# Kernel optimization log

Measured on AMD Instinct MI355X. Metric: run time of the kernel, lower is better.

The kernel has to match this reference:

```python
import jax, jax.numpy as jnp
import numpy as np

B, H, V, DEPTH = 64, 1024, 32000, 5


def setup_inputs() -> dict:
    key = jax.random.key(0)
    ks = jax.random.split(key, 9)
    s = 1.0 / np.sqrt(H)
    u = lambda k, shape: jax.random.uniform(k, shape, jnp.float32, -s, s)
    return {
        "encoding": jax.random.normal(ks[0], (B, H), jnp.float32),
        "Whh_l": u(ks[1], (3 * H, H)),
        "bih_l": u(ks[2], (3 * H,)),
        "bhh_l": u(ks[3], (3 * H,)),
        "Whh_r": u(ks[4], (3 * H, H)),
        "bih_r": u(ks[5], (3 * H,)),
        "bhh_r": u(ks[6], (3 * H,)),
        "W_out": u(ks[7], (V, H)),
        "b_out": u(ks[8], (V,)),
        "depth": DEPTH,
    }


def _gru_zero_input(h, Whh, bih, bhh):
    # PyTorch GRU cell with x == 0: W_ih @ x vanishes, only b_ih survives.
    d = h.shape[-1]
    gh = h @ Whh.T + bhh                                   # [N, 3H]
    r = jax.nn.sigmoid(bih[:d] + gh[..., :d])
    z = jax.nn.sigmoid(bih[d:2 * d] + gh[..., d:2 * d])
    n = jnp.tanh(bih[2 * d:] + r * gh[..., 2 * d:])
    return (1.0 - z) * n + z * h


def reference(encoding, Whh_l, bih_l, bhh_l, Whh_r, bih_r, bhh_r, W_out, b_out, depth):
    b, h = encoding.shape
    cur = encoding[:, None, :]                             # [B, 1, H] roots
    for _ in range(depth):                                 # expand perfect binary tree, level-batched
        n = cur.shape[1]
        flat = cur.reshape(b * n, h)
        left = _gru_zero_input(flat, Whh_l, bih_l, bhh_l).reshape(b, n, h)
        right = _gru_zero_input(flat, Whh_r, bih_r, bhh_r).reshape(b, n, h)
        cur = jnp.stack([left, right], axis=2).reshape(b, 2 * n, h)  # interleave children
    logits = jnp.einsum("blh,vh->blv", cur, W_out) + b_out  # [B, L, V]
    return jax.nn.log_softmax(logits, axis=-1)
```

## Files before the change

### kernel.cpp

```cpp
#include <hip/hip_runtime.h>
#include <hip/hip_bf16.h>
#include <cstdint>
#include <cstddef>

#define H_DIM   1024
#define B_DIM   64
#define V_DIM   32000
#define DEPTH_C 5

using bf16x8  = __attribute__((ext_vector_type(8))) __bf16;
using bf16x4  = __attribute__((ext_vector_type(4))) __bf16;
using floatx4 = __attribute__((ext_vector_type(4))) float;

__device__ __forceinline__ void gl_lds16(const __bf16* g, __bf16* l) {
  __builtin_amdgcn_global_load_lds(
      (const __attribute__((address_space(1))) unsigned int*)g,
      (__attribute__((address_space(3))) unsigned int*)l, 16, 0, 0);
}

__global__ __launch_bounds__(256) void f2b(const float* __restrict__ in,
                                           __bf16* __restrict__ out, int n) {
  for (int i = (blockIdx.x * 256 + threadIdx.x) * 4; i < n;
       i += gridDim.x * 1024) {
    float4 v = *(const float4*)(in + i);
    bf16x4 o;
    o[0] = (__bf16)v.x; o[1] = (__bf16)v.y; o[2] = (__bf16)v.z; o[3] = (__bf16)v.w;
    *(bf16x4*)(out + i) = o;
  }
}

__device__ __forceinline__ bf16x8 cvt8(float4 a, float4 b) {
  bf16x8 r;
  r[0] = (__bf16)a.x; r[1] = (__bf16)a.y; r[2] = (__bf16)a.z; r[3] = (__bf16)a.w;
  r[4] = (__bf16)b.x; r[5] = (__bf16)b.y; r[6] = (__bf16)b.z; r[7] = (__bf16)b.w;
  return r;
}

#define VMCNT(n) asm volatile("s_waitcnt vmcnt(" #n ")" ::: "memory")
#define LGK0()                                  \
  do {                                          \
    asm volatile("s_waitcnt lgkmcnt(0)" ::: "memory"); \
    __builtin_amdgcn_sched_barrier(0);          \
  } while (0)
#define SBAR()                                  \
  do {                                          \
    __builtin_amdgcn_sched_barrier(0);          \
    __builtin_amdgcn_s_barrier();               \
    __builtin_amdgcn_sched_barrier(0);          \
  } while (0)
#define LDA(MH, KS)                                                          \
  do {                                                                       \
    _Pragma("unroll") for (int mf = 0; mf < 4; ++mf)                         \
        aF[mf] = *(const bf16x8*)(cb + aRow + (MH)*8192 + mf * 2048 +        \
                                  ((KS) ? cksw1 : cksw0));                   \
  } while (0)
#define LDB(KS)                                                              \
  do {                                                                       \
    _Pragma("unroll") for (int nj = 0; nj < 4; ++nj)                         \
        bB[nj] = *(const bf16x8*)(cb + 32768 + bRow + nj * 2048 +            \
                                  ((KS) ? cksw1 : cksw0));                   \
  } while (0)
#define MM(MH)                                                               \
  do {                                                                       \
    __builtin_amdgcn_s_setprio(1);                                           \
    _Pragma("unroll") for (int mf = 0; mf < 4; ++mf)                         \
        _Pragma("unroll") for (int nj = 0; nj < 4; ++nj)                     \
            acc[(MH)*4 + mf][nj] = __builtin_amdgcn_mfma_f32_16x16x32_bf16(  \
                aF[mf], bB[nj], acc[(MH)*4 + mf][nj], 0, 0, 0);              \
    __builtin_amdgcn_s_setprio(0);                                           \
  } while (0)

__global__ __launch_bounds__(512, 2) void gemm_logits_8ph(
    const __bf16* __restrict__ A, const __bf16* __restrict__ Wb,
    float* __restrict__ Cf, const float* __restrict__ bias,
    float2* __restrict__ part) {
  __shared__ __align__(16) char smem[131072];

  const int tid = threadIdx.x;
  int h = blockIdx.y * 8 + blockIdx.x;
  h = (h & 7) * 125 + (h >> 3);
  const int bx = h & 7, by = h >> 3;
  const int m0 = bx * 256, n0 = by * 256;

  const int lane = tid & 63, wave = tid >> 6;
  const int wr = wave >> 2, wc = wave & 3;
  const int lrow = lane & 15, quad = lane >> 4;

  const int aRow  = (wr * 128 + lrow) * 128;
  const int bRow  = (wc * 64 + lrow) * 128;
  const int lsw   = (lrow & 7) << 4;
  const int cksw0 = (quad * 16) ^ lsw;
  const int cksw1 = (64 + quad * 16) ^ lsw;

  const int t8  = tid >> 3;
  const int cix = (tid & 7) ^ (t8 & 7);
  const __bf16* gA00 = A + (size_t)(m0 + t8) * 1024 + cix * 8;
  const __bf16* gA01 = A + (size_t)(m0 + 128 + t8) * 1024 + cix * 8;
  const __bf16* gA10 = gA00 + 64 * 1024;
  const __bf16* gA11 = gA01 + 64 * 1024;
  const __bf16* gB00 = Wb + (size_t)(n0 + t8) * 1024 + cix * 8;
  const __bf16* gB01 = Wb + (size_t)(n0 + 64 + t8) * 1024 + cix * 8;
  const __bf16* gB10 = gB00 + 128 * 1024;
  const __bf16* gB11 = gB01 + 128 * 1024;

  floatx4 acc[8][4] = {};
  bf16x8 aF[4], bB[4];

  gl_lds16(gA00, (__bf16*)(smem + tid * 16));
  gl_lds16(gA01, (__bf16*)(smem + 16384 + tid * 16));
  gl_lds16(gB00, (__bf16*)(smem + 32768 + tid * 16));
  gl_lds16(gB01, (__bf16*)(smem + 40960 + tid * 16));
  gl_lds16(gB10, (__bf16*)(smem + 49152 + tid * 16));
  gl_lds16(gB11, (__bf16*)(smem + 57344 + tid * 16));
  gl_lds16(gA10, (__bf16*)(smem + 8192 + tid * 16));
  gl_lds16(gA11, (__bf16*)(smem + 24576 + tid * 16));
  VMCNT(2);
  SBAR();

  for (int t = 0; t < 15; ++t) {
    char* cb = smem + (t & 1) * 65536;
    char* nb = smem + ((t & 1) ^ 1) * 65536;
    const int ke = (t + 1) * 64;
    LDB(0); LDA(0, 0);
    gl_lds16(gA00 + ke, (__bf16*)(nb + tid * 16));
    gl_lds16(gA01 + ke, (__bf16*)(nb + 16384 + tid * 16));
    SBAR(); LGK0();
    MM(0);
    VMCNT(2); SBAR();
    LDA(1, 0);
    gl_lds16(gB00 + ke, (__bf16*)(nb + 32768 + tid * 16));
    gl_lds16(gB01 + ke, (__bf16*)(nb + 40960 + tid * 16));
    SBAR(); LGK0();
    MM(1);
    SBAR();
    LDB(1); LDA(0, 1);
    gl_lds16(gB10 + ke, (__bf16*)(nb + 49152 + tid * 16));
    gl_lds16(gB11 + ke, (__bf16*)(nb + 57344 + tid * 16));
    SBAR(); LGK0();
    MM(0);
    SBAR();
    LDA(1, 1);
    gl_lds16(gA10 + ke, (__bf16*)(nb + 8192 + tid * 16));
    gl_lds16(gA11 + ke, (__bf16*)(nb + 24576 + tid * 16));
    SBAR(); LGK0();
    MM(1);
    VMCNT(2); SBAR();
  }
  {
    char* cb = smem + 65536;
    LDB(0); LDA(0, 0); MM(0);
    VMCNT(0); SBAR();
    LDA(1, 0); MM(1);
    LDB(1); LDA(0, 1); MM(0);
    LDA(1, 1); MM(1);
  }

  float bv[4];
#pragma unroll
  for (int nj = 0; nj < 4; ++nj) bv[nj] = bias[n0 + wc * 64 + nj * 16 + lrow];

  float* lf = (float*)smem;

  __syncthreads();
#pragma unroll
  for (int half = 0; half < 2; ++half) {
    if (half) __syncthreads();
    if (wr == half) {
#pragma unroll
      for (int mi = 0; mi < 8; ++mi) {
#pragma unroll
        for (int nj = 0; nj < 4; ++nj) {
          const int colg = wc * 16 + nj * 4 + (lrow >> 2);
          const int cole = lrow & 3;
#pragma unroll
          for (int r = 0; r < 4; ++r) {
            const int rowL = mi * 16 + quad * 4 + r;
            lf[rowL * 256 + ((colg ^ (rowL & 7)) << 2) + cole] =
                acc[mi][nj][r] + bv[nj];
          }
        }
      }
    }
    __syncthreads();
#pragma unroll
    for (int it = 0; it < 16; ++it) {
      const int rowL = it * 8 + wave;
      const int rsw  = rowL & 7;
      const float4 v =
          *(const float4*)&lf[rowL * 256 + ((lane ^ rsw) << 2)];
      const int grow = m0 + half * 128 + rowL;
      *(float4*)(Cf + (size_t)grow * V_DIM + n0 + lane * 4) = v;
      float mx = fmaxf(fmaxf(v.x, v.y), fmaxf(v.z, v.w));
#pragma unroll
      for (int off = 32; off; off >>= 1) mx = fmaxf(mx, __shfl_xor(mx, off, 64));
      float sm = __expf(v.x - mx) + __expf(v.y - mx) + __expf(v.z - mx) +
                 __expf(v.w - mx);
#pragma unroll
      for (int off = 32; off; off >>= 1) sm += __shfl_xor(sm, off, 64);
      if (lane == 0)
        part[(size_t)grow * gridDim.y + by] = make_float2(mx, sm);
    }
  }
}

__global__ __launch_bounds__(256) void gemm_tree(
    const __bf16* __restrict__ A, const __bf16* __restrict__ Wb0,
    const __bf16* __restrict__ Wb1, __bf16* __restrict__ Cb, int M) {
  constexpr int K = H_DIM;
  __shared__ __align__(16) __bf16 As[3][128 * 32];
  __shared__ __align__(16) __bf16 Bs[3][64 * 32];

  const int tid = threadIdx.x;
  const int nbx = gridDim.x;
  const int nwg = nbx * gridDim.y;
  int hflat = blockIdx.y * nbx + blockIdx.x;
  if ((nwg & 7) == 0) {
    const int cpx = nwg >> 3;
    hflat = (hflat & 7) * cpx + (hflat >> 3);
  }
  const int bx = hflat % nbx;
  const int by = hflat / nbx;
  const int m0 = bx * 128;
  const int n0 = by * 64;
  const int lane = tid & 63, wave = tid >> 6;
  const int lrow = lane & 15, quad = lane >> 4;
  const int wm = wave * 32;

  const __bf16* Wb = Wb0;
  int nw0 = n0;
  if (n0 >= 3072) { Wb = Wb1; nw0 = n0 - 3072; }

  const int sr = tid >> 2;
  const int sk = (tid & 3) * 8;
  int ra0 = m0 + sr;      if (ra0 >= M) ra0 = M - 1;
  int ra1 = m0 + sr + 64; if (ra1 >= M) ra1 = M - 1;
  const __bf16* ga0 = A + (size_t)ra0 * K + sk;
  const __bf16* ga1 = A + (size_t)ra1 * K + sk;
  const __bf16* gb0 = Wb + (size_t)(nw0 + sr) * K + sk;

  floatx4 acc[2][4] = {};

#define TSTAGE(T, BUF)                                     \
  do {                                                     \
    gl_lds16(ga0 + (T) * 32, As[BUF] + tid * 8);           \
    gl_lds16(ga1 + (T) * 32, As[BUF] + 2048 + tid * 8);    \
    gl_lds16(gb0 + (T) * 32, Bs[BUF] + tid * 8);           \
  } while (0)
#define TCOMP(CB)                                                            \
  do {                                                                       \
    bf16x8 af[2], bfr[4];                                                    \
    _Pragma("unroll") for (int i = 0; i < 2; i++)                            \
        af[i] = *(const bf16x8*)(&As[CB][(wm + i * 16 + lrow) * 32 +         \
                                         quad * 8]);                         \
    _Pragma("unroll") for (int j = 0; j < 4; j++)                            \
        bfr[j] = *(const bf16x8*)(&Bs[CB][(j * 16 + lrow) * 32 + quad * 8]); \
    _Pragma("unroll") for (int i = 0; i < 2; i++)                            \
        _Pragma("unroll") for (int j = 0; j < 4; j++)                        \
            acc[i][j] = __builtin_amdgcn_mfma_f32_16x16x32_bf16(             \
                af[i], bfr[j], acc[i][j], 0, 0, 0);                          \
  } while (0)

  TSTAGE(0, 0);
  TSTAGE(1, 1);
  for (int t = 0; t < 31; ++t) {
    VMCNT(3);
    SBAR();
    if (t + 2 < 32) TSTAGE(t + 2, (t + 2) % 3);
    TCOMP(t % 3);
  }
  VMCNT(0);
  SBAR();
  TCOMP(31 % 3);
#undef TSTAGE
#undef TCOMP

#pragma unroll
  for (int i = 0; i < 2; i++) {
#pragma unroll
    for (int j = 0; j < 4; j++) {
      const int col = n0 + j * 16 + lrow;
#pragma unroll
      for (int r = 0; r < 4; r++) {
        const int row = m0 + wm + i * 16 + quad * 4 + r;
        if (row < M) Cb[(size_t)row * 6144 + col] = (__bf16)acc[i][j][r];
      }
    }
  }
}

template <int TN, bool LOGITS, bool WBF16>
__global__ __launch_bounds__(256) void gemm_nt(
    const __bf16* __restrict__ A, const __bf16* __restrict__ Wb0,
    const __bf16* __restrict__ Wb1, const float* __restrict__ Wf,
    __bf16* __restrict__ Cb, float* __restrict__ Cf,
    const float* __restrict__ bias, float2* __restrict__ part, int M, int N) {
  constexpr int K = H_DIM;
  constexpr int MI = (TN == 128) ? 4 : 2;
  __shared__ __align__(16) __bf16 As[128 * 32];
  __shared__ __align__(16) __bf16 Bs[TN * 32];

  const int tid  = threadIdx.x;
  const int nbx = gridDim.x;
  const int nwg = nbx * gridDim.y;
  int hflat = blockIdx.y * nbx + blockIdx.x;
  if ((nwg & 7) == 0) {
    const int cpx = nwg >> 3;
    hflat = (hflat & 7) * cpx + (hflat >> 3);
  }
  const int bx = hflat % nbx;
  const int by = hflat / nbx;
  const int m0   = bx * 128;
  const int n0   = by * TN;
  const int lane = tid & 63;
  const int wave = tid >> 6;
  const int lrow = lane & 15;
  const int quad = lane >> 4;
  const int wm   = (TN == 128) ? (wave >> 1) * 64 : wave * 32;
  const int wn   = (TN == 128) ? (wave & 1) * 64 : 0;

  const __bf16* Wb = Wb0;
  int nw0 = n0;
  if (!LOGITS && n0 >= 3072) { Wb = Wb1; nw0 = n0 - 3072; }

  const int sr = tid >> 2;
  const int sk = (tid & 3) * 8;

  int ra0 = m0 + sr;      if (ra0 >= M) ra0 = M - 1;
  int ra1 = m0 + sr + 64; if (ra1 >= M) ra1 = M - 1;
  const __bf16* ga0 = A + (size_t)ra0 * K + sk;
  const __bf16* ga1 = A + (size_t)ra1 * K + sk;
  const __bf16* gb0 = nullptr; const __bf16* gb1 = nullptr;
  const float* gf0 = nullptr; const float* gf1 = nullptr;
  if (WBF16) {
    gb0 = Wb + (size_t)(nw0 + sr) * K + sk;
    if (TN == 128) gb1 = Wb + (size_t)(nw0 + sr + 64) * K + sk;
  } else {
    gf0 = Wf + (size_t)(n0 + sr) * K + sk;
    gf1 = Wf + (size_t)(n0 + sr + 64) * K + sk;
  }

  floatx4 acc[MI][4] = {};

  for (int kt = 0; kt < K; kt += 32) {
    float4 w00, w01, w10, w11;
    if (!WBF16) {
      w00 = *(const float4*)(gf0 + kt);
      w01 = *(const float4*)(gf0 + kt + 4);
      w10 = *(const float4*)(gf1 + kt);
      w11 = *(const float4*)(gf1 + kt + 4);
    }
    __syncthreads();
    gl_lds16(ga0 + kt, As + tid * 8);
    gl_lds16(ga1 + kt, As + 2048 + tid * 8);
    if (WBF16) {
      gl_lds16(gb0 + kt, Bs + tid * 8);
      if (TN == 128) gl_lds16(gb1 + kt, Bs + 2048 + tid * 8);
    } else {
      *(bf16x8*)(&Bs[sr * 32 + sk])        = cvt8(w00, w01);
      *(bf16x8*)(&Bs[(sr + 64) * 32 + sk]) = cvt8(w10, w11);
    }
    __syncthreads();

    bf16x8 af[MI], bfr[4];
#pragma unroll
    for (int i = 0; i < MI; i++)
      af[i] = *(const bf16x8*)(&As[(wm + i * 16 + lrow) * 32 + quad * 8]);
#pragma unroll
    for (int j = 0; j < 4; j++)
      bfr[j] = *(const bf16x8*)(&Bs[(wn + j * 16 + lrow) * 32 + quad * 8]);
#pragma unroll
    for (int i = 0; i < MI; i++)
#pragma unroll
      for (int j = 0; j < 4; j++)
        acc[i][j] =
            __builtin_amdgcn_mfma_f32_16x16x32_bf16(af[i], bfr[j], acc[i][j], 0, 0, 0);
  }

  float bv[4];
  if constexpr (LOGITS) {
#pragma unroll
    for (int j = 0; j < 4; j++) bv[j] = bias[n0 + wn + j * 16 + lrow];
  }
#pragma unroll
  for (int i = 0; i < MI; i++) {
#pragma unroll
    for (int j = 0; j < 4; j++) {
      const int col = n0 + wn + j * 16 + lrow;
#pragma unroll
      for (int r = 0; r < 4; r++) {
        const int row = m0 + wm + i * 16 + quad * 4 + r;
        if (row < M) {
          if (LOGITS) Cf[(size_t)row * N + col] = acc[i][j][r] + bv[j];
          else        Cb[(size_t)row * N + col] = (__bf16)acc[i][j][r];
        }
      }
    }
  }

  if constexpr (LOGITS) {
    __shared__ float pmax[2][128], psum[2][128];
    const int wnh = wn >> 6;
#pragma unroll
    for (int i = 0; i < MI; i++) {
#pragma unroll
      for (int r = 0; r < 4; r++) {
        float mx = -3.0e38f;
#pragma unroll
        for (int j = 0; j < 4; j++) mx = fmaxf(mx, acc[i][j][r] + bv[j]);
#pragma unroll
        for (int mask = 1; mask < 16; mask <<= 1)
          mx = fmaxf(mx, __shfl_xor(mx, mask, 64));
        float sm = 0.f;
#pragma unroll
        for (int j = 0; j < 4; j++) sm += __expf(acc[i][j][r] + bv[j] - mx);
#pragma unroll
        for (int mask = 1; mask < 16; mask <<= 1)
          sm += __shfl_xor(sm, mask, 64);
        if (lrow == 0) {
          pmax[wnh][wm + i * 16 + quad * 4 + r] = mx;
          psum[wnh][wm + i * 16 + quad * 4 + r] = sm;
        }
      }
    }
    __syncthreads();
    if (tid < 128) {
      const float ma = pmax[0][tid], mb = pmax[1][tid];
      const float nm = fmaxf(ma, mb);
      const float ns = psum[0][tid] * __expf(ma - nm) +
                       psum[1][tid] * __expf(mb - nm);
      part[(size_t)(m0 + tid) * gridDim.y + by] = make_float2(nm, ns);
    }
  }
}

__global__ __launch_bounds__(256) void gru_gate(
    const __bf16* __restrict__ gh, const float* __restrict__ bih_l,
    const float* __restrict__ bhh_l, const float* __restrict__ bih_r,
    const float* __restrict__ bhh_r, const __bf16* __restrict__ hin,
    __bf16* __restrict__ hout, int n) {
  const int row = blockIdx.x;
  const int c = threadIdx.x * 4;
  const int b = row / n, j = row - b * n;
  const size_t g6 = (size_t)row * 6144;
  const bf16x4 h4 = *(const bf16x4*)(hin + (size_t)row * H_DIM + c);
  const size_t obase = (size_t)(b * 2 * n + 2 * j) * H_DIM;

  bf16x4 og[2];
#pragma unroll
  for (int side = 0; side < 2; ++side) {
    const float* bih = side ? bih_r : bih_l;
    const float* bhh = side ? bhh_r : bhh_l;
    const size_t gb = g6 + side * 3072;
    const bf16x4 g0 = *(const bf16x4*)(gh + gb + c);
    const bf16x4 g1 = *(const bf16x4*)(gh + gb + 1024 + c);
    const bf16x4 g2 = *(const bf16x4*)(gh + gb + 2048 + c);
    const float4 br0 = *(const float4*)(bih + c);
    const float4 br1 = *(const float4*)(bih + 1024 + c);
    const float4 br2 = *(const float4*)(bih + 2048 + c);
    const float4 bh0 = *(const float4*)(bhh + c);
    const float4 bh1 = *(const float4*)(bhh + 1024 + c);
    const float4 bh2 = *(const float4*)(bhh + 2048 + c);
    const float* pr0 = (const float*)&br0; const float* ph0 = (const float*)&bh0;
    const float* pr1 = (const float*)&br1; const float* ph1 = (const float*)&bh1;
    const float* pr2 = (const float*)&br2; const float* ph2 = (const float*)&bh2;
    bf16x4 o;
#pragma unroll
    for (int e = 0; e < 4; ++e) {
      const float gr = (float)g0[e] + ph0[e];
      const float gz = (float)g1[e] + ph1[e];
      const float gn = (float)g2[e] + ph2[e];
      const float r = 1.f / (1.f + __expf(-(pr0[e] + gr)));
      const float z = 1.f / (1.f + __expf(-(pr1[e] + gz)));
      const float nn = tanhf(pr2[e] + r * gn);
      o[e] = (__bf16)((1.f - z) * nn + z * (float)h4[e]);
    }
    og[side] = o;
  }
  *(bf16x4*)(hout + obase + c) = og[0];
  *(bf16x4*)(hout + obase + H_DIM + c) = og[1];
}

__global__ __launch_bounds__(256) void lsm_finish(
    float* __restrict__ out, const float2* __restrict__ part, int nb) {
  const int row = blockIdx.x;
  const int tid = threadIdx.x;

  float m = -3.0e38f, s = 0.f;
  if (tid < nb) {
    const float2 p = part[(size_t)row * nb + tid];
    m = p.x; s = p.y;
  }
#pragma unroll
  for (int off = 32; off; off >>= 1) {
    float om = __shfl_xor(m, off, 64);
    float os = __shfl_xor(s, off, 64);
    float nm = fmaxf(m, om);
    s = s * __expf(m - nm) + os * __expf(om - nm);
    m = nm;
  }
  __shared__ float rm[4], rs[4];
  if ((tid & 63) == 0) { rm[tid >> 6] = m; rs[tid >> 6] = s; }
  __syncthreads();
  const float M4 = fmaxf(fmaxf(rm[0], rm[1]), fmaxf(rm[2], rm[3]));
  const float S4 = rs[0] * __expf(rm[0] - M4) + rs[1] * __expf(rm[1] - M4) +
                   rs[2] * __expf(rm[2] - M4) + rs[3] * __expf(rm[3] - M4);
  const float lg = M4 + __logf(S4);

  float4* p4 = (float4*)(out + (size_t)row * V_DIM);
  for (int i = tid; i < 8000; i += 256) {
    float4 v = p4[i];
    v.x -= lg; v.y -= lg; v.z -= lg; v.w -= lg;
    p4[i] = v;
  }
}

extern "C" void kernel_launch(void* const* d_in, const int* in_sizes, int n_in,
                              void* d_out, int out_size, void* d_ws,
                              size_t ws_size, hipStream_t stream) {
  const float* enc   = (const float*)d_in[0];
  const float* Whh_l = (const float*)d_in[1];
  const float* bih_l = (const float*)d_in[2];
  const float* bhh_l = (const float*)d_in[3];
  const float* Whh_r = (const float*)d_in[4];
  const float* bih_r = (const float*)d_in[5];
  const float* bhh_r = (const float*)d_in[6];
  const float* W_out = (const float*)d_in[7];
  const float* b_out = (const float*)d_in[8];
  float* out = (float*)d_out;

  char* ws = (char*)d_ws;
  __bf16* ghb    = (__bf16*)ws;
  __bf16* buf0   = (__bf16*)(ws + 12582912);
  __bf16* buf1   = (__bf16*)(ws + 16777216);
  __bf16* WhhB_l = (__bf16*)(ws + 20971520);
  __bf16* WhhB_r = WhhB_l + 3145728;
  __bf16* encB   = (__bf16*)(ws + 33554432);
  __bf16* WoutB  = (__bf16*)(ws + 33685504);
  float2* part   = (float2*)ghb;
  const bool big = ws_size >= (size_t)(33685504 + 65536000);

  f2b<<<256, 256, 0, stream>>>(Whh_l, WhhB_l, 3 * H_DIM * H_DIM);
  f2b<<<256, 256, 0, stream>>>(Whh_r, WhhB_r, 3 * H_DIM * H_DIM);
  f2b<<<64, 256, 0, stream>>>(enc, encB, B_DIM * H_DIM);
  if (big) f2b<<<1024, 256, 0, stream>>>(W_out, WoutB, V_DIM * H_DIM);

  const __bf16* cur = encB;
  __bf16* nxt = buf0;
  int n = 1;
  for (int d = 0; d < DEPTH_C; d++) {
    const int M = B_DIM * n;
    dim3 gg((M + 127) / 128, 6144 / 64);
    gemm_tree<<<gg, 256, 0, stream>>>(cur, WhhB_l, WhhB_r, ghb, M);
    gru_gate<<<dim3(M), 256, 0, stream>>>(ghb, bih_l, bhh_l, bih_r, bhh_r,
                                          cur, nxt, n);
    cur = nxt;
    nxt = (nxt == buf0) ? buf1 : buf0;
    n *= 2;
  }

  if (big) {
    gemm_logits_8ph<<<dim3(8, 125), 512, 0, stream>>>(cur, WoutB, out, b_out,
                                                      part);
    lsm_finish<<<2048, 256, 0, stream>>>(out, part, 125);
  } else {
    dim3 gf(2048 / 128, V_DIM / 128);
    gemm_nt<128, true, false><<<gf, 256, 0, stream>>>(
        cur, nullptr, nullptr, W_out, nullptr, out, b_out, part, 2048, V_DIM);
    lsm_finish<<<2048, 256, 0, stream>>>(out, part, 250);
  }
}
```

Before: 749.0 us.

## Prefetch B tiles earlier and write logits directly from registers with in-wave softmax partials

Reorders the global-to-LDS prefetches in the output GEMM main loop so B sub-tiles are issued alongside A sub-tiles earlier, with the vmcnt wait loosened accordingly, to give loads more time to land. The epilogue no longer stages the accumulator tile through LDS. Logits are stored straight from registers, per-row max/sum partials are reduced with 16-lane shuffles and merged across the four column waves through a small LDS buffer. This removes two LDS round trips and their barriers, at the cost of scalar, less coalesced global stores of the logits.

```diff
diff --git a/kernel.cpp b/kernel.cpp
--- a/kernel.cpp
+++ b/kernel.cpp
@@ -124,24 +124,24 @@
     LDB(0); LDA(0, 0);
     gl_lds16(gA00 + ke, (__bf16*)(nb + tid * 16));
     gl_lds16(gA01 + ke, (__bf16*)(nb + 16384 + tid * 16));
+    gl_lds16(gB00 + ke, (__bf16*)(nb + 32768 + tid * 16));
+    gl_lds16(gB01 + ke, (__bf16*)(nb + 40960 + tid * 16));
     SBAR(); LGK0();
     MM(0);
-    VMCNT(2); SBAR();
+    VMCNT(4); SBAR();
     LDA(1, 0);
-    gl_lds16(gB00 + ke, (__bf16*)(nb + 32768 + tid * 16));
-    gl_lds16(gB01 + ke, (__bf16*)(nb + 40960 + tid * 16));
+    gl_lds16(gB10 + ke, (__bf16*)(nb + 49152 + tid * 16));
+    gl_lds16(gB11 + ke, (__bf16*)(nb + 57344 + tid * 16));
     SBAR(); LGK0();
     MM(1);
     SBAR();
     LDB(1); LDA(0, 1);
-    gl_lds16(gB10 + ke, (__bf16*)(nb + 49152 + tid * 16));
-    gl_lds16(gB11 + ke, (__bf16*)(nb + 57344 + tid * 16));
+    gl_lds16(gA10 + ke, (__bf16*)(nb + 8192 + tid * 16));
+    gl_lds16(gA11 + ke, (__bf16*)(nb + 24576 + tid * 16));
     SBAR(); LGK0();
     MM(0);
     SBAR();
     LDA(1, 1);
-    gl_lds16(gA10 + ke, (__bf16*)(nb + 8192 + tid * 16));
-    gl_lds16(gA11 + ke, (__bf16*)(nb + 24576 + tid * 16));
     SBAR(); LGK0();
     MM(1);
     VMCNT(2); SBAR();
@@ -159,47 +159,48 @@
 #pragma unroll
   for (int nj = 0; nj < 4; ++nj) bv[nj] = bias[n0 + wc * 64 + nj * 16 + lrow];
 
-  float* lf = (float*)smem;
-
+  float* pm = (float*)smem;
+  float* ps = (float*)(smem + 4096);
+
+#pragma unroll
+  for (int mi = 0; mi < 8; ++mi) {
+    const int rowb = wr * 128 + mi * 16 + quad * 4;
+#pragma unroll
+    for (int r = 0; r < 4; ++r) {
+      const float v0 = acc[mi][0][r] + bv[0];
+      const float v1 = acc[mi][1][r] + bv[1];
+      const float v2 = acc[mi][2][r] + bv[2];
+      const float v3 = acc[mi][3][r] + bv[3];
+      const size_t rb = (size_t)(m0 + rowb + r) * V_DIM + n0 + wc * 64 + lrow;
+      Cf[rb]      = v0;
+      Cf[rb + 16] = v1;
+      Cf[rb + 32] = v2;
+      Cf[rb + 48] = v3;
+      float mx = fmaxf(fmaxf(v0, v1), fmaxf(v2, v3));
+#pragma unroll
+      for (int msk = 1; msk < 16; msk <<= 1)
+        mx = fmaxf(mx, __shfl_xor(mx, msk, 64));
+      float sm = __expf(v0 - mx) + __expf(v1 - mx) + __expf(v2 - mx) +
+                 __expf(v3 - mx);
+#pragma unroll
+      for (int msk = 1; msk < 16; msk <<= 1) sm += __shfl_xor(sm, msk, 64);
+      if (lrow == 0) {
+        pm[(rowb + r) * 4 + wc] = mx;
+        ps[(rowb + r) * 4 + wc] = sm;
+      }
+    }
+  }
   __syncthreads();
-#pragma unroll
-  for (int half = 0; half < 2; ++half) {
-    if (half) __syncthreads();
-    if (wr == half) {
-#pragma unroll
-      for (int mi = 0; mi < 8; ++mi) {
-#pragma unroll
-        for (int nj = 0; nj < 4; ++nj) {
-          const int colg = wc * 16 + nj * 4 + (lrow >> 2);
-          const int cole = lrow & 3;
-#pragma unroll
-          for (int r = 0; r < 4; ++r) {
-            const int rowL = mi * 16 + quad * 4 + r;
-            lf[rowL * 256 + ((colg ^ (rowL & 7)) << 2) + cole] =
-                acc[mi][nj][r] + bv[nj];
-          }
-        }
-      }
-    }
-    __syncthreads();
-#pragma unroll
-    for (int it = 0; it < 16; ++it) {
-      const int rowL = it * 8 + wave;
-      const int rsw  = rowL & 7;
-      const float4 v =
-          *(const float4*)&lf[rowL * 256 + ((lane ^ rsw) << 2)];
-      const int grow = m0 + half * 128 + rowL;
-      *(float4*)(Cf + (size_t)grow * V_DIM + n0 + lane * 4) = v;
-      float mx = fmaxf(fmaxf(v.x, v.y), fmaxf(v.z, v.w));
-#pragma unroll
-      for (int off = 32; off; off >>= 1) mx = fmaxf(mx, __shfl_xor(mx, off, 64));
-      float sm = __expf(v.x - mx) + __expf(v.y - mx) + __expf(v.z - mx) +
-                 __expf(v.w - mx);
-#pragma unroll
-      for (int off = 32; off; off >>= 1) sm += __shfl_xor(sm, off, 64);
-      if (lane == 0)
-        part[(size_t)grow * gridDim.y + by] = make_float2(mx, sm);
-    }
+  if (tid < 256) {
+    float m = pm[tid * 4], s = ps[tid * 4];
+#pragma unroll
+    for (int w = 1; w < 4; ++w) {
+      const float om = pm[tid * 4 + w], os = ps[tid * 4 + w];
+      const float nm = fmaxf(m, om);
+      s = s * __expf(m - nm) + os * __expf(om - nm);
+      m = nm;
+    }
+    part[(size_t)(m0 + tid) * gridDim.y + by] = make_float2(m, s);
   }
 }
 
```

New measurement: 723.7 us. 3.4% less time.
